# Kernel tuning notes

Hardware: AMD Instinct MI355X
Metric: run time of the kernel (lower is better)

Reference implementation:

```python
import jax, jax.numpy as jnp
import numpy as np

B, C_IN, H, W = 2, 256, 64, 64
D, NH, WS = 128, 8, 8          # embed_dim, num_heads, window_size
N_PTS = 8192
CAP = 256                      # max tokens per window (64 pixels + points, padded)
ODE_STEPS = 4                  # fixed-step RK4 approximating dopri5 on t in [0,1]


def setup_inputs() -> dict:
    key = jax.random.key(0)
    ks = jax.random.split(key, 16)
    p = lambda k, shape, fan: (jax.random.normal(k, shape, jnp.float32) / np.float32(np.sqrt(fan)))
    return {
        "in_image_feat": jax.random.normal(ks[0], (B, C_IN, H, W), jnp.float32),
        "pts_uv": jax.random.randint(ks[1], (N_PTS, 3), 0, 64),
        "pts_feat": jax.random.normal(ks[2], (N_PTS, D), jnp.float32),
        "conv_in_w": p(ks[3], (D, C_IN), C_IN),         # conv256_128 (1x1)
        "conv_in_b": jnp.zeros((D,), jnp.float32),
        "qkv_w": p(ks[4], (3 * D, D), D),               # sptr attn qkv
        "qkv_b": jnp.zeros((3 * D,), jnp.float32),
        "attnproj_w": p(ks[5], (D, D), D),              # sptr attn out proj
        "attnproj_b": jnp.zeros((D,), jnp.float32),
        "ode_w": p(ks[6], (D, D), D),                   # outimagefc128_128_ode
        "ode_b": jnp.zeros((D,), jnp.float32),
        "conv_out_w": p(ks[7], (C_IN, D), D),           # conv128_256 (1x1)
        "conv_out_b": jnp.zeros((C_IN,), jnp.float32),
    }


def _windowed_attention(feat, wid, NW, qkv_w, qkv_b, proj_w, proj_b):
    """Var-length windowed MHSA (sptr.VarLengthMultiheadSA) via pad-to-CAP."""
    T, d = feat.shape
    hd = d // NH
    order = jnp.argsort(wid)                      # stable sort by window id
    wid_s, feat_s = wid[order], feat[order]
    counts = jax.ops.segment_sum(jnp.ones_like(wid), wid, num_segments=NW)
    starts = jnp.cumsum(counts) - counts
    rank = jnp.arange(T) - starts[wid_s]          # within-window position
    valid = rank < CAP
    wid_w = jnp.where(valid, wid_s, NW)           # overflow -> dummy window
    rank_w = jnp.where(valid, rank, 0)
    buf = jnp.zeros((NW + 1, CAP, d), feat.dtype).at[wid_w, rank_w].set(feat_s)
    msk = jnp.zeros((NW + 1, CAP), bool).at[wid_w, rank_w].set(valid)
    qkv = buf @ qkv_w.T + qkv_b                   # [NW+1, CAP, 3d]
    q, k, v = (t.reshape(NW + 1, CAP, NH, hd) for t in jnp.split(qkv, 3, axis=-1))
    scores = jnp.einsum('wqhd,wkhd->whqk', q, k) / np.float32(np.sqrt(hd))
    scores = jnp.where(msk[:, None, None, :], scores, jnp.float32(-1e9))
    attn = jax.nn.softmax(scores, axis=-1)
    o = jnp.einsum('whqk,wkhd->wqhd', attn, v).reshape(NW + 1, CAP, d)
    o = o @ proj_w.T + proj_b
    out_s = jnp.where(valid[:, None], o[wid_w, rank_w], feat_s)
    return jnp.zeros_like(out_s).at[order].set(out_s)  # unsort


def reference(in_image_feat, pts_uv, pts_feat, conv_in_w, conv_in_b,
              qkv_w, qkv_b, attnproj_w, attnproj_b,
              ode_w, ode_b, conv_out_w, conv_out_b):
    b, c, h, w = in_image_feat.shape
    d = conv_in_w.shape[0]
    # 1x1 conv 256->128
    x = jnp.einsum('bchw,ec->bhwe', in_image_feat, conv_in_w) + conv_in_b
    pix_feat = x.reshape(b * h * w, d)
    # pixel uv grid (convert_image_to_uv): flatten order (b, h, w); u=w idx, v=h idx
    vv, uu = jnp.meshgrid(jnp.arange(h), jnp.arange(w), indexing='ij')
    pix_b = jnp.repeat(jnp.arange(b), h * w)
    pix_u = jnp.tile(uu.reshape(-1), b)
    pix_v = jnp.tile(vv.reshape(-1), b)
    # projected point uv (convert_pts_to_uv result, made in-range)
    pts_b = pts_uv[:, 0] % b
    pts_u = pts_uv[:, 1] % w
    pts_v = pts_uv[:, 2] % h
    tok_b = jnp.concatenate([pix_b, pts_b])
    tok_u = jnp.concatenate([pix_u, pts_u])
    tok_v = jnp.concatenate([pix_v, pts_v])
    feat = jnp.concatenate([pix_feat, pts_feat], axis=0)
    nwx, nwy = w // WS, h // WS
    wid = (tok_b * nwy + tok_v // WS) * nwx + tok_u // WS
    NW = b * nwx * nwy
    out = _windowed_attention(feat, wid, NW, qkv_w, qkv_b, attnproj_w, attnproj_b)
    img = out[: b * h * w]
    # fcode branch: odeint(ODEFunc(Linear), t=[0,1]) ~ fixed-step RK4, + residual
    f = lambda y: jax.nn.relu(y @ ode_w.T + ode_b)
    dt = jnp.float32(1.0 / ODE_STEPS)
    y = img
    for _ in range(ODE_STEPS):
        k1 = f(y); k2 = f(y + 0.5 * dt * k1); k3 = f(y + 0.5 * dt * k2); k4 = f(y + dt * k3)
        y = y + (dt / 6.0) * (k1 + 2.0 * k2 + 2.0 * k3 + k4)
    img = y + img
    # 1x1 conv 128->256 back to image layout
    img = img.reshape(b, h, w, d)
    return jnp.einsum('bhwd,cd->bchw', img, conv_out_w) + conv_out_b[None, :, None, None]
```

## Files before the change

kernel.cpp:

```cpp
#include <hip/hip_runtime.h>

typedef short bf16x8 __attribute__((ext_vector_type(8)));
typedef float f32x4 __attribute__((ext_vector_type(4)));

__device__ __forceinline__ float b2f(unsigned short s) {
    union { float f; unsigned u; } x; x.u = ((unsigned)s) << 16; return x.f;
}
__device__ __forceinline__ unsigned short f2b(float f) {
    unsigned u = __float_as_uint(f);
    unsigned r = (u + 0x7fffu + ((u >> 16) & 1u)) >> 16;
    return (unsigned short)r;
}

__global__ __launch_bounds__(256) void cast_k(const float* __restrict__ ciw,
                                              const float* __restrict__ qw,
                                              const float* __restrict__ pw,
                                              const float* __restrict__ ow,
                                              const float* __restrict__ cw,
                                              const float* __restrict__ ptsf,
                                              unsigned short* __restrict__ dst,
                                              int* __restrict__ cnt) {
    if (blockIdx.x == 0 && threadIdx.x < 128) cnt[threadIdx.x] = 0;
    int i = blockIdx.x * 256 + threadIdx.x;
    float v;
    if (i < 32768)        v = ciw[i];
    else if (i < 81920)   v = qw[i - 32768];
    else if (i < 98304)   v = pw[i - 81920];
    else if (i < 114688)  v = ow[i - 98304];
    else if (i < 147456)  v = cw[i - 114688];
    else                  v = ptsf[i - 147456];
    dst[i] = f2b(v);
}

__global__ __launch_bounds__(256) void transpose_k(const float* __restrict__ in,
                                                   unsigned short* __restrict__ out) {
    __shared__ unsigned short t[64][65];
    int p0 = blockIdx.x * 64, c0 = blockIdx.y * 64, b = blockIdx.z;
    int lane = threadIdx.x & 63, quad = threadIdx.x >> 6;
#pragma unroll
    for (int i = 0; i < 16; ++i) {
        int c = quad + i * 4;
        t[c][lane] = f2b(in[((size_t)(b * 256 + c0 + c)) * 4096 + p0 + lane]);
    }
    __syncthreads();
#pragma unroll
    for (int i = 0; i < 16; ++i) {
        int p = quad + i * 4;
        out[((size_t)(b * 4096 + p0 + p)) * 256 + c0 + lane] = t[lane][p];
    }
}

__global__ __launch_bounds__(256) void assign_k(const int* __restrict__ uv,
                                                int* __restrict__ cnt,
                                                int* __restrict__ wpts) {
    int i = blockIdx.x * 256 + threadIdx.x;
    if (i >= 8192) return;
    int b = uv[3 * i] & 1;
    int u = uv[3 * i + 1] & 63;
    int v = uv[3 * i + 2] & 63;
    int w = b * 64 + ((v >> 3) << 3) + (u >> 3);
    int slot = atomicAdd(cnt + w, 1);
    if (slot < 192) wpts[w * 192 + slot] = i;
}

template<int K, int MODE>
__global__ __launch_bounds__(256) void gemm_k(const unsigned short* __restrict__ A0,
                                              const unsigned short* __restrict__ A1,
                                              const unsigned short* __restrict__ Wm,
                                              const float* __restrict__ bias,
                                              void* __restrict__ Cv, int ldc) {
    int lane = threadIdx.x & 63;
    int wv = threadIdx.x >> 6;
    int m0 = (blockIdx.x * 4 + wv) * 16;
    int q = lane & 15, g = lane >> 4;
    const unsigned short* Arow;
    {
        int row = m0 + q;
        Arow = (A1 != nullptr && row >= 8192) ? (A1 + (size_t)(row - 8192) * K)
                                              : (A0 + (size_t)row * K);
    }
    int nb = blockIdx.y * 64;
    int koff = g * 8;
    f32x4 acc[4];
#pragma unroll
    for (int t = 0; t < 4; ++t) acc[t] = (f32x4){0.f, 0.f, 0.f, 0.f};
#pragma unroll
    for (int k0 = 0; k0 < K; k0 += 32) {
        bf16x8 a = *(const bf16x8*)(Arow + k0 + koff);
#pragma unroll
        for (int t = 0; t < 4; ++t) {
            const unsigned short* wr = Wm + (size_t)(nb + t * 16 + q) * K + k0 + koff;
            bf16x8 bfr = *(const bf16x8*)wr;
            acc[t] = __builtin_amdgcn_mfma_f32_16x16x32_bf16(a, bfr, acc[t], 0, 0, 0);
        }
    }
#pragma unroll
    for (int t = 0; t < 4; ++t) {
        int n = nb + t * 16 + q;
        float bs = bias[n];
        if constexpr (MODE == 2) {
            int p = m0 + g * 4;
            float4 pk;
            pk.x = acc[t][0] + bs;
            pk.y = acc[t][1] + bs;
            pk.z = acc[t][2] + bs;
            pk.w = acc[t][3] + bs;
            size_t ad = ((size_t)((p >> 12) * 256 + n)) * 4096 + (size_t)(p & 4095);
            *(float4*)((float*)Cv + ad) = pk;
        } else {
#pragma unroll
            for (int rr = 0; rr < 4; ++rr) {
                float v = acc[t][rr] + bs;
                int row = m0 + g * 4 + rr;
                if constexpr (MODE == 0)
                    ((unsigned short*)Cv)[(size_t)row * ldc + n] = f2b(v);
                else
                    ((float*)Cv)[(size_t)row * ldc + n] = v;
            }
        }
    }
}

__global__ __launch_bounds__(256) void attn_k(const unsigned short* __restrict__ qkv,
                                              const int* __restrict__ cnt,
                                              const int* __restrict__ wpts,
                                              unsigned short* __restrict__ aout) {
    __shared__ unsigned short Kl[256][24];
    __shared__ unsigned short Vt[16][264];
    int blk = blockIdx.x;
    int w = blk >> 3, h = blk & 7;
    int b = w >> 6, wy = (w >> 3) & 7, wx = w & 7;
    int tid = threadIdx.x, wave = tid >> 6, lane = tid & 63;
    int q = lane & 15, g = lane >> 4;
    int c = cnt[w]; if (c > 192) c = 192;
    int T = 64 + c;

    {
        int t = tid;
        if (t < T) {
            int tok;
            if (t < 64) tok = b * 4096 + (wy * 8 + (t >> 3)) * 64 + wx * 8 + (t & 7);
            else        tok = 8192 + wpts[w * 192 + t - 64];
            const unsigned short* base = qkv + (size_t)tok * 384 + h * 16;
            bf16x8 k0 = *(const bf16x8*)(base + 128);
            bf16x8 v0 = *(const bf16x8*)(base + 256);
            *(bf16x8*)&Kl[t][0] = k0;
#pragma unroll
            for (int d = 0; d < 8; ++d) Vt[d][t] = (unsigned short)v0[d];
            bf16x8 k1 = *(const bf16x8*)(base + 136);
            bf16x8 v1 = *(const bf16x8*)(base + 264);
            *(bf16x8*)&Kl[t][8] = k1;
#pragma unroll
            for (int d = 0; d < 8; ++d) Vt[8 + d][t] = (unsigned short)v1[d];
        } else {
            bf16x8 z;
#pragma unroll
            for (int d = 0; d < 8; ++d) z[d] = 0;
            *(bf16x8*)&Kl[t][0] = z;
            *(bf16x8*)&Kl[t][8] = z;
#pragma unroll
            for (int d = 0; d < 16; ++d) Vt[d][t] = 0;
        }
    }

    int qq = wave * 16 + q;
    int qrow = b * 4096 + (wy * 8 + (qq >> 3)) * 64 + wx * 8 + (qq & 7);
    bf16x8 qfrag;
#pragma unroll
    for (int j = 0; j < 8; ++j) qfrag[j] = 0;
    if (g < 2) qfrag = *(const bf16x8*)(qkv + (size_t)qrow * 384 + h * 16 + g * 8);

    __syncthreads();

    float p[16][4];
    int MT = (T + 15) >> 4;
#pragma unroll
    for (int mt = 0; mt < 16; ++mt) {
        if (mt < MT) {
            bf16x8 af = *(const bf16x8*)&Kl[mt * 16 + q][(g & 1) * 8];
            f32x4 cc = (f32x4){0.f, 0.f, 0.f, 0.f};
            cc = __builtin_amdgcn_mfma_f32_16x16x32_bf16(af, qfrag, cc, 0, 0, 0);
#pragma unroll
            for (int r = 0; r < 4; ++r) {
                int tok = mt * 16 + g * 4 + r;
                p[mt][r] = (tok < T) ? cc[r] * 0.25f : -1e30f;
            }
        } else {
#pragma unroll
            for (int r = 0; r < 4; ++r) p[mt][r] = -1e30f;
        }
    }

    float mv = -3.0e38f;
#pragma unroll
    for (int mt = 0; mt < 16; ++mt)
#pragma unroll
        for (int r = 0; r < 4; ++r) mv = fmaxf(mv, p[mt][r]);
    mv = fmaxf(mv, __shfl_xor(mv, 16));
    mv = fmaxf(mv, __shfl_xor(mv, 32));
    float ls = 0.f;
#pragma unroll
    for (int mt = 0; mt < 16; ++mt)
#pragma unroll
        for (int r = 0; r < 4; ++r) {
            float e = __expf(p[mt][r] - mv);
            p[mt][r] = e;
            ls += e;
        }
    ls += __shfl_xor(ls, 16);
    ls += __shfl_xor(ls, 32);

    f32x4 oacc = (f32x4){0.f, 0.f, 0.f, 0.f};
    int KS = (T + 31) >> 5;
    int srcA = q + (((2 * g) & 3) << 4);
    int srcB = q + (((2 * g + 1) & 3) << 4);
#pragma unroll
    for (int ks = 0; ks < 8; ++ks) {
        if (ks < KS) {
            int n0lo, n0hi, n1lo, n1hi;
            asm("v_cvt_pk_bf16_f32 %0, %1, %2" : "=v"(n0lo) : "v"(p[2 * ks][0]), "v"(p[2 * ks][1]));
            asm("v_cvt_pk_bf16_f32 %0, %1, %2" : "=v"(n0hi) : "v"(p[2 * ks][2]), "v"(p[2 * ks][3]));
            asm("v_cvt_pk_bf16_f32 %0, %1, %2" : "=v"(n1lo) : "v"(p[2 * ks + 1][0]), "v"(p[2 * ks + 1][1]));
            asm("v_cvt_pk_bf16_f32 %0, %1, %2" : "=v"(n1hi) : "v"(p[2 * ks + 1][2]), "v"(p[2 * ks + 1][3]));
            int a0 = __shfl(n0lo, srcA), b0 = __shfl(n1lo, srcA);
            int a1 = __shfl(n0hi, srcA), b1 = __shfl(n1hi, srcA);
            int a2 = __shfl(n0lo, srcB), b2 = __shfl(n1lo, srcB);
            int a3 = __shfl(n0hi, srcB), b3 = __shfl(n1hi, srcB);
            union { int d[4]; bf16x8 v; } pb;
            bool lo2 = (g < 2);
            pb.d[0] = lo2 ? a0 : b0;
            pb.d[1] = lo2 ? a1 : b1;
            pb.d[2] = lo2 ? a2 : b2;
            pb.d[3] = lo2 ? a3 : b3;
            bf16x8 vf = *(const bf16x8*)&Vt[q][ks * 32 + g * 8];
            oacc = __builtin_amdgcn_mfma_f32_16x16x32_bf16(vf, pb.v, oacc, 0, 0, 0);
        }
    }

    float inv = 1.0f / ls;
    ushort4 st;
    st.x = f2b(oacc[0] * inv);
    st.y = f2b(oacc[1] * inv);
    st.z = f2b(oacc[2] * inv);
    st.w = f2b(oacc[3] * inv);
    *(ushort4*)(aout + (size_t)qrow * 128 + h * 16 + g * 4) = st;
}

__global__ __launch_bounds__(128) void ode_k(const float* __restrict__ img,
                                             const unsigned short* __restrict__ Wg,
                                             const float* __restrict__ bg,
                                             unsigned short* __restrict__ outimg) {
    __shared__ unsigned short Wl[128][136];
    __shared__ unsigned short tc[2][16][136];
    int tid = threadIdx.x, wave = tid >> 6, lane = tid & 63;
    int g = lane >> 4, q = lane & 15;
    {
        int part = tid & 15;
#pragma unroll
        for (int it = 0; it < 16; ++it) {
            int rr = (tid >> 4) + it * 8;
            *(bf16x8*)&Wl[rr][part * 8] = *(const bf16x8*)(Wg + rr * 128 + part * 8);
        }
    }
    int R0 = blockIdx.x * 32 + wave * 16;
    float bs[8];
#pragma unroll
    for (int tn = 0; tn < 8; ++tn) bs[tn] = bg[tn * 16 + q];
    float y[32], acc[32], ko[32];
#pragma unroll
    for (int tn = 0; tn < 8; ++tn)
#pragma unroll
        for (int rr = 0; rr < 4; ++rr)
            y[tn * 4 + rr] = img[(size_t)(R0 + g * 4 + rr) * 128 + tn * 16 + q];

#define WRITE_TC(EXPR)                                            \
    {                                                             \
        _Pragma("unroll")                                         \
        for (int tn = 0; tn < 8; ++tn) {                          \
            _Pragma("unroll")                                     \
            for (int rr = 0; rr < 4; ++rr) {                      \
                int i_ = tn * 4 + rr;                             \
                tc[wave][g * 4 + rr][tn * 16 + q] = f2b(EXPR);    \
            }                                                     \
        }                                                         \
        __syncthreads();                                          \
    }

#define EVAL()                                                                         \
    {                                                                                  \
        bf16x8 af[4];                                                                  \
        _Pragma("unroll")                                                              \
        for (int tk = 0; tk < 4; ++tk)                                                 \
            af[tk] = *(const bf16x8*)&tc[wave][q][tk * 32 + g * 8];                    \
        _Pragma("unroll")                                                              \
        for (int tn = 0; tn < 8; ++tn) {                                               \
            f32x4 cc = (f32x4){0.f, 0.f, 0.f, 0.f};                                    \
            _Pragma("unroll")                                                          \
            for (int tk = 0; tk < 4; ++tk) {                                           \
                bf16x8 bfr = *(const bf16x8*)&Wl[tn * 16 + q][tk * 32 + g * 8];        \
                cc = __builtin_amdgcn_mfma_f32_16x16x32_bf16(af[tk], bfr, cc, 0, 0, 0);\
            }                                                                          \
            _Pragma("unroll")                                                          \
            for (int rr = 0; rr < 4; ++rr)                                             \
                ko[tn * 4 + rr] = fmaxf(cc[rr] + bs[tn], 0.f);                         \
        }                                                                              \
    }

    WRITE_TC(y[i_])
    const float dt = 0.25f;
    for (int st = 0; st < 4; ++st) {
        EVAL();
#pragma unroll
        for (int i = 0; i < 32; ++i) acc[i] = y[i] + (dt / 6.f) * ko[i];
        WRITE_TC(y[i_] + (0.5f * dt) * ko[i_])
        EVAL();
#pragma unroll
        for (int i = 0; i < 32; ++i) acc[i] += (dt / 3.f) * ko[i];
        WRITE_TC(y[i_] + (0.5f * dt) * ko[i_])
        EVAL();
#pragma unroll
        for (int i = 0; i < 32; ++i) acc[i] += (dt / 3.f) * ko[i];
        WRITE_TC(y[i_] + dt * ko[i_])
        EVAL();
#pragma unroll
        for (int i = 0; i < 32; ++i) y[i] = acc[i] + (dt / 6.f) * ko[i];
        WRITE_TC(y[i_])
    }
#pragma unroll
    for (int tn = 0; tn < 8; ++tn)
#pragma unroll
        for (int rr = 0; rr < 4; ++rr) {
            size_t idx = (size_t)(R0 + g * 4 + rr) * 128 + tn * 16 + q;
            outimg[idx] = f2b(y[tn * 4 + rr] + img[idx]);
        }
#undef WRITE_TC
#undef EVAL
}

extern "C" void kernel_launch(void* const* d_in, const int* in_sizes, int n_in,
                              void* d_out, int out_size, void* d_ws, size_t ws_size,
                              hipStream_t stream) {
    (void)in_sizes; (void)n_in; (void)out_size; (void)ws_size;
    const float* img_in = (const float*)d_in[0];
    const int*   pts_uv = (const int*)d_in[1];
    const float* ptsf   = (const float*)d_in[2];
    const float* ciw    = (const float*)d_in[3];
    const float* cib    = (const float*)d_in[4];
    const float* qw     = (const float*)d_in[5];
    const float* qb     = (const float*)d_in[6];
    const float* pw     = (const float*)d_in[7];
    const float* pb     = (const float*)d_in[8];
    const float* ow     = (const float*)d_in[9];
    const float* ob     = (const float*)d_in[10];
    const float* cw     = (const float*)d_in[11];
    const float* cb     = (const float*)d_in[12];

    char* ws = (char*)d_ws;
    unsigned short* Arm  = (unsigned short*)(ws);
    unsigned short* feat = (unsigned short*)(ws + 4194304);
    unsigned short* qkv  = (unsigned short*)(ws + 6291456);
    unsigned short* aout = (unsigned short*)(ws + 18874368);
    float*          img0 = (float*)(ws + 20971520);
    unsigned short* imgf = (unsigned short*)(ws + 25165824);
    int*            cnt  = (int*)(ws + 27262976);
    int*            wpts = (int*)(ws + 27263488);
    unsigned short* wb   = (unsigned short*)(ws + 27787264);
    unsigned short* ciw_b = wb;
    unsigned short* qw_b  = wb + 32768;
    unsigned short* pw_b  = wb + 81920;
    unsigned short* ow_b  = wb + 98304;
    unsigned short* cw_b  = wb + 114688;
    unsigned short* ptsf_b= wb + 147456;

    cast_k<<<4672, 256, 0, stream>>>(ciw, qw, pw, ow, cw, ptsf, wb, cnt);
    transpose_k<<<dim3(64, 4, 2), 256, 0, stream>>>(img_in, Arm);
    assign_k<<<32, 256, 0, stream>>>(pts_uv, cnt, wpts);
    gemm_k<256, 0><<<dim3(128, 2), 256, 0, stream>>>(Arm, nullptr, ciw_b, cib, feat, 128);
    gemm_k<128, 0><<<dim3(256, 6), 256, 0, stream>>>(feat, ptsf_b, qw_b, qb, qkv, 384);
    attn_k<<<1024, 256, 0, stream>>>(qkv, cnt, wpts, aout);
    gemm_k<128, 1><<<dim3(128, 2), 256, 0, stream>>>(aout, nullptr, pw_b, pb, img0, 128);
    ode_k<<<256, 128, 0, stream>>>(img0, ow_b, ob, imgf);
    gemm_k<128, 2><<<dim3(128, 4), 256, 0, stream>>>(imgf, nullptr, cw_b, cb, d_out, 0);
}
```

Measured before the change: 170.5 us.

## Fuse transpose into conv-in GEMM and fuse proj+ODE+conv-out into one tail kernel

Folds the NCHW-to-row transpose into the input 1x1 conv kernel through shared memory, converts point features to bf16 inside the QKV GEMM instead of in a separate cast pass, and merges the attention output projection, the RK4 ODE and the output 1x1 conv into a single per-row-block kernel. This removes several launches and the intermediate global buffers (transposed image, fp32 img0, bf16 imgf). In exchange the fused kernels run fewer blocks (128 and 256) and carry more registers, which can lower occupancy. Tail-kernel weights are read directly from global memory.

```diff
diff --git a/kernel.cpp b/kernel.cpp
--- a/kernel.cpp
+++ b/kernel.cpp
@@ -17,7 +17,6 @@
                                               const float* __restrict__ pw,
                                               const float* __restrict__ ow,
                                               const float* __restrict__ cw,
-                                              const float* __restrict__ ptsf,
                                               unsigned short* __restrict__ dst,
                                               int* __restrict__ cnt) {
     if (blockIdx.x == 0 && threadIdx.x < 128) cnt[threadIdx.x] = 0;
@@ -27,27 +26,8 @@
     else if (i < 81920)   v = qw[i - 32768];
     else if (i < 98304)   v = pw[i - 81920];
     else if (i < 114688)  v = ow[i - 98304];
-    else if (i < 147456)  v = cw[i - 114688];
-    else                  v = ptsf[i - 147456];
+    else                  v = cw[i - 114688];
     dst[i] = f2b(v);
-}
-
-__global__ __launch_bounds__(256) void transpose_k(const float* __restrict__ in,
-                                                   unsigned short* __restrict__ out) {
-    __shared__ unsigned short t[64][65];
-    int p0 = blockIdx.x * 64, c0 = blockIdx.y * 64, b = blockIdx.z;
-    int lane = threadIdx.x & 63, quad = threadIdx.x >> 6;
-#pragma unroll
-    for (int i = 0; i < 16; ++i) {
-        int c = quad + i * 4;
-        t[c][lane] = f2b(in[((size_t)(b * 256 + c0 + c)) * 4096 + p0 + lane]);
-    }
-    __syncthreads();
-#pragma unroll
-    for (int i = 0; i < 16; ++i) {
-        int p = quad + i * 4;
-        out[((size_t)(b * 4096 + p0 + p)) * 256 + c0 + lane] = t[lane][p];
-    }
 }
 
 __global__ __launch_bounds__(256) void assign_k(const int* __restrict__ uv,
@@ -63,61 +43,93 @@
     if (slot < 192) wpts[w * 192 + slot] = i;
 }
 
-template<int K, int MODE>
-__global__ __launch_bounds__(256) void gemm_k(const unsigned short* __restrict__ A0,
-                                              const unsigned short* __restrict__ A1,
-                                              const unsigned short* __restrict__ Wm,
-                                              const float* __restrict__ bias,
-                                              void* __restrict__ Cv, int ldc) {
-    int lane = threadIdx.x & 63;
-    int wv = threadIdx.x >> 6;
+__global__ __launch_bounds__(256) void cin_k(const float* __restrict__ in,
+                                             const unsigned short* __restrict__ Wm,
+                                             const float* __restrict__ bias,
+                                             unsigned short* __restrict__ feat) {
+    __shared__ unsigned short t[64][65];
+    __shared__ unsigned short At[64][264];
+    int p0 = blockIdx.x * 64, b = p0 >> 12, hw0 = p0 & 4095;
+    int lane = threadIdx.x & 63, quad = threadIdx.x >> 6;
+    for (int j = 0; j < 4; ++j) {
+        int c0 = j * 64;
+#pragma unroll
+        for (int i = 0; i < 16; ++i) {
+            int c = quad + i * 4;
+            t[c][lane] = f2b(in[((size_t)(b * 256 + c0 + c)) * 4096 + hw0 + lane]);
+        }
+        __syncthreads();
+#pragma unroll
+        for (int i = 0; i < 16; ++i) {
+            int p = quad + i * 4;
+            At[p][c0 + lane] = t[lane][p];
+        }
+        __syncthreads();
+    }
+    int q = lane & 15, g = lane >> 4;
+    int m0 = quad * 16;
+    f32x4 acc[8];
+#pragma unroll
+    for (int tn = 0; tn < 8; ++tn) acc[tn] = (f32x4){0.f, 0.f, 0.f, 0.f};
+#pragma unroll
+    for (int k0 = 0; k0 < 256; k0 += 32) {
+        bf16x8 a = *(const bf16x8*)&At[m0 + q][k0 + g * 8];
+#pragma unroll
+        for (int tn = 0; tn < 8; ++tn) {
+            bf16x8 bfr = *(const bf16x8*)(Wm + (size_t)(tn * 16 + q) * 256 + k0 + g * 8);
+            acc[tn] = __builtin_amdgcn_mfma_f32_16x16x32_bf16(a, bfr, acc[tn], 0, 0, 0);
+        }
+    }
+#pragma unroll
+    for (int tn = 0; tn < 8; ++tn) {
+        int n = tn * 16 + q;
+        float bs = bias[n];
+#pragma unroll
+        for (int rr = 0; rr < 4; ++rr)
+            feat[(size_t)(p0 + m0 + g * 4 + rr) * 128 + n] = f2b(acc[tn][rr] + bs);
+    }
+}
+
+__global__ __launch_bounds__(256) void qkv_k(const unsigned short* __restrict__ feat,
+                                             const float* __restrict__ ptsf,
+                                             const unsigned short* __restrict__ Wm,
+                                             const float* __restrict__ bias,
+                                             unsigned short* __restrict__ qkv) {
+    int lane = threadIdx.x & 63, wv = threadIdx.x >> 6;
     int m0 = (blockIdx.x * 4 + wv) * 16;
     int q = lane & 15, g = lane >> 4;
-    const unsigned short* Arow;
-    {
-        int row = m0 + q;
-        Arow = (A1 != nullptr && row >= 8192) ? (A1 + (size_t)(row - 8192) * K)
-                                              : (A0 + (size_t)row * K);
-    }
-    int nb = blockIdx.y * 64;
-    int koff = g * 8;
+    int nb = blockIdx.y * 64, koff = g * 8;
+    bool isPt = m0 >= 8192;
     f32x4 acc[4];
 #pragma unroll
-    for (int t = 0; t < 4; ++t) acc[t] = (f32x4){0.f, 0.f, 0.f, 0.f};
-#pragma unroll
-    for (int k0 = 0; k0 < K; k0 += 32) {
-        bf16x8 a = *(const bf16x8*)(Arow + k0 + koff);
-#pragma unroll
-        for (int t = 0; t < 4; ++t) {
-            const unsigned short* wr = Wm + (size_t)(nb + t * 16 + q) * K + k0 + koff;
-            bf16x8 bfr = *(const bf16x8*)wr;
-            acc[t] = __builtin_amdgcn_mfma_f32_16x16x32_bf16(a, bfr, acc[t], 0, 0, 0);
-        }
-    }
-#pragma unroll
-    for (int t = 0; t < 4; ++t) {
-        int n = nb + t * 16 + q;
+    for (int tt = 0; tt < 4; ++tt) acc[tt] = (f32x4){0.f, 0.f, 0.f, 0.f};
+#pragma unroll
+    for (int k0 = 0; k0 < 128; k0 += 32) {
+        bf16x8 a;
+        if (isPt) {
+            const float* pr = ptsf + (size_t)(m0 + q - 8192) * 128 + k0 + koff;
+            float4 f0 = *(const float4*)pr;
+            float4 f1 = *(const float4*)(pr + 4);
+            a[0] = (short)f2b(f0.x); a[1] = (short)f2b(f0.y);
+            a[2] = (short)f2b(f0.z); a[3] = (short)f2b(f0.w);
+            a[4] = (short)f2b(f1.x); a[5] = (short)f2b(f1.y);
+            a[6] = (short)f2b(f1.z); a[7] = (short)f2b(f1.w);
+        } else {
+            a = *(const bf16x8*)(feat + (size_t)(m0 + q) * 128 + k0 + koff);
+        }
+#pragma unroll
+        for (int tt = 0; tt < 4; ++tt) {
+            bf16x8 bfr = *(const bf16x8*)(Wm + (size_t)(nb + tt * 16 + q) * 128 + k0 + koff);
+            acc[tt] = __builtin_amdgcn_mfma_f32_16x16x32_bf16(a, bfr, acc[tt], 0, 0, 0);
+        }
+    }
+#pragma unroll
+    for (int tt = 0; tt < 4; ++tt) {
+        int n = nb + tt * 16 + q;
         float bs = bias[n];
-        if constexpr (MODE == 2) {
-            int p = m0 + g * 4;
-            float4 pk;
-            pk.x = acc[t][0] + bs;
-            pk.y = acc[t][1] + bs;
-            pk.z = acc[t][2] + bs;
-            pk.w = acc[t][3] + bs;
-            size_t ad = ((size_t)((p >> 12) * 256 + n)) * 4096 + (size_t)(p & 4095);
-            *(float4*)((float*)Cv + ad) = pk;
-        } else {
-#pragma unroll
-            for (int rr = 0; rr < 4; ++rr) {
-                float v = acc[t][rr] + bs;
-                int row = m0 + g * 4 + rr;
-                if constexpr (MODE == 0)
-                    ((unsigned short*)Cv)[(size_t)row * ldc + n] = f2b(v);
-                else
-                    ((float*)Cv)[(size_t)row * ldc + n] = v;
-            }
-        }
+#pragma unroll
+        for (int rr = 0; rr < 4; ++rr)
+            qkv[(size_t)(m0 + g * 4 + rr) * 384 + n] = f2b(acc[tt][rr] + bs);
     }
 }
 
@@ -134,7 +146,6 @@
     int q = lane & 15, g = lane >> 4;
     int c = cnt[w]; if (c > 192) c = 192;
     int T = 64 + c;
-
     {
         int t = tid;
         if (t < T) {
@@ -162,7 +173,6 @@
             for (int d = 0; d < 16; ++d) Vt[d][t] = 0;
         }
     }
-
     int qq = wave * 16 + q;
     int qrow = b * 4096 + (wy * 8 + (qq >> 3)) * 64 + wx * 8 + (qq & 7);
     bf16x8 qfrag;
@@ -190,7 +200,6 @@
             for (int r = 0; r < 4; ++r) p[mt][r] = -1e30f;
         }
     }
-
     float mv = -3.0e38f;
 #pragma unroll
     for (int mt = 0; mt < 16; ++mt)
@@ -236,7 +245,6 @@
             oacc = __builtin_amdgcn_mfma_f32_16x16x32_bf16(vf, pb.v, oacc, 0, 0, 0);
         }
     }
-
     float inv = 1.0f / ls;
     ushort4 st;
     st.x = f2b(oacc[0] * inv);
@@ -246,10 +254,14 @@
     *(ushort4*)(aout + (size_t)qrow * 128 + h * 16 + g * 4) = st;
 }
 
-__global__ __launch_bounds__(128) void ode_k(const float* __restrict__ img,
-                                             const unsigned short* __restrict__ Wg,
-                                             const float* __restrict__ bg,
-                                             unsigned short* __restrict__ outimg) {
+__global__ __launch_bounds__(128) void tail_k(const unsigned short* __restrict__ aout,
+                                              const unsigned short* __restrict__ pwb,
+                                              const float* __restrict__ pb,
+                                              const unsigned short* __restrict__ owb,
+                                              const float* __restrict__ ob,
+                                              const unsigned short* __restrict__ cwb,
+                                              const float* __restrict__ cb,
+                                              float* __restrict__ outp) {
     __shared__ unsigned short Wl[128][136];
     __shared__ unsigned short tc[2][16][136];
     int tid = threadIdx.x, wave = tid >> 6, lane = tid & 63;
@@ -259,19 +271,40 @@
 #pragma unroll
         for (int it = 0; it < 16; ++it) {
             int rr = (tid >> 4) + it * 8;
-            *(bf16x8*)&Wl[rr][part * 8] = *(const bf16x8*)(Wg + rr * 128 + part * 8);
+            *(bf16x8*)&Wl[rr][part * 8] = *(const bf16x8*)(owb + rr * 128 + part * 8);
         }
     }
     int R0 = blockIdx.x * 32 + wave * 16;
+
+    float y0[32];
+    {
+        const unsigned short* Arow = aout + (size_t)(R0 + q) * 128;
+        f32x4 pacc[8];
+#pragma unroll
+        for (int tn = 0; tn < 8; ++tn) pacc[tn] = (f32x4){0.f, 0.f, 0.f, 0.f};
+#pragma unroll
+        for (int k0 = 0; k0 < 128; k0 += 32) {
+            bf16x8 a = *(const bf16x8*)(Arow + k0 + g * 8);
+#pragma unroll
+            for (int tn = 0; tn < 8; ++tn) {
+                bf16x8 bfr = *(const bf16x8*)(pwb + (size_t)(tn * 16 + q) * 128 + k0 + g * 8);
+                pacc[tn] = __builtin_amdgcn_mfma_f32_16x16x32_bf16(a, bfr, pacc[tn], 0, 0, 0);
+            }
+        }
+#pragma unroll
+        for (int tn = 0; tn < 8; ++tn) {
+            float bs = pb[tn * 16 + q];
+#pragma unroll
+            for (int rr = 0; rr < 4; ++rr) y0[tn * 4 + rr] = pacc[tn][rr] + bs;
+        }
+    }
+
     float bs[8];
 #pragma unroll
-    for (int tn = 0; tn < 8; ++tn) bs[tn] = bg[tn * 16 + q];
+    for (int tn = 0; tn < 8; ++tn) bs[tn] = ob[tn * 16 + q];
     float y[32], acc[32], ko[32];
 #pragma unroll
-    for (int tn = 0; tn < 8; ++tn)
-#pragma unroll
-        for (int rr = 0; rr < 4; ++rr)
-            y[tn * 4 + rr] = img[(size_t)(R0 + g * 4 + rr) * 128 + tn * 16 + q];
+    for (int i = 0; i < 32; ++i) y[i] = y0[i];
 
 #define WRITE_TC(EXPR)                                            \
     {                                                             \
@@ -326,13 +359,30 @@
         for (int i = 0; i < 32; ++i) y[i] = acc[i] + (dt / 6.f) * ko[i];
         WRITE_TC(y[i_])
     }
-#pragma unroll
-    for (int tn = 0; tn < 8; ++tn)
-#pragma unroll
-        for (int rr = 0; rr < 4; ++rr) {
-            size_t idx = (size_t)(R0 + g * 4 + rr) * 128 + tn * 16 + q;
-            outimg[idx] = f2b(y[tn * 4 + rr] + img[idx]);
-        }
+
+    WRITE_TC(y[i_] + y0[i_])
+    {
+        int p = R0 + g * 4;
+        int bb = p >> 12, plo = p & 4095;
+#pragma unroll
+        for (int tn2 = 0; tn2 < 16; ++tn2) {
+            f32x4 cc = (f32x4){0.f, 0.f, 0.f, 0.f};
+#pragma unroll
+            for (int tk = 0; tk < 4; ++tk) {
+                bf16x8 af = *(const bf16x8*)&tc[wave][q][tk * 32 + g * 8];
+                bf16x8 bfr = *(const bf16x8*)(cwb + (size_t)(tn2 * 16 + q) * 128 + tk * 32 + g * 8);
+                cc = __builtin_amdgcn_mfma_f32_16x16x32_bf16(af, bfr, cc, 0, 0, 0);
+            }
+            int ch = tn2 * 16 + q;
+            float bsv = cb[ch];
+            float4 stv;
+            stv.x = cc[0] + bsv;
+            stv.y = cc[1] + bsv;
+            stv.z = cc[2] + bsv;
+            stv.w = cc[3] + bsv;
+            *(float4*)(outp + ((size_t)(bb * 256 + ch)) * 4096 + plo) = stv;
+        }
+    }
 #undef WRITE_TC
 #undef EVAL
 }
@@ -356,29 +406,22 @@
     const float* cb     = (const float*)d_in[12];
 
     char* ws = (char*)d_ws;
-    unsigned short* Arm  = (unsigned short*)(ws);
-    unsigned short* feat = (unsigned short*)(ws + 4194304);
-    unsigned short* qkv  = (unsigned short*)(ws + 6291456);
-    unsigned short* aout = (unsigned short*)(ws + 18874368);
-    float*          img0 = (float*)(ws + 20971520);
-    unsigned short* imgf = (unsigned short*)(ws + 25165824);
-    int*            cnt  = (int*)(ws + 27262976);
-    int*            wpts = (int*)(ws + 27263488);
-    unsigned short* wb   = (unsigned short*)(ws + 27787264);
+    unsigned short* feat = (unsigned short*)(ws);
+    unsigned short* qkv  = (unsigned short*)(ws + 2097152);
+    unsigned short* aout = (unsigned short*)(ws + 14680064);
+    int*            cnt  = (int*)(ws + 16777216);
+    int*            wpts = (int*)(ws + 16777728);
+    unsigned short* wb   = (unsigned short*)(ws + 16876544);
     unsigned short* ciw_b = wb;
     unsigned short* qw_b  = wb + 32768;
     unsigned short* pw_b  = wb + 81920;
     unsigned short* ow_b  = wb + 98304;
     unsigned short* cw_b  = wb + 114688;
-    unsigned short* ptsf_b= wb + 147456;
-
-    cast_k<<<4672, 256, 0, stream>>>(ciw, qw, pw, ow, cw, ptsf, wb, cnt);
-    transpose_k<<<dim3(64, 4, 2), 256, 0, stream>>>(img_in, Arm);
+
+    cast_k<<<576, 256, 0, stream>>>(ciw, qw, pw, ow, cw, wb, cnt);
     assign_k<<<32, 256, 0, stream>>>(pts_uv, cnt, wpts);
-    gemm_k<256, 0><<<dim3(128, 2), 256, 0, stream>>>(Arm, nullptr, ciw_b, cib, feat, 128);
-    gemm_k<128, 0><<<dim3(256, 6), 256, 0, stream>>>(feat, ptsf_b, qw_b, qb, qkv, 384);
+    cin_k<<<128, 256, 0, stream>>>(img_in, ciw_b, cib, feat);
+    qkv_k<<<dim3(256, 6), 256, 0, stream>>>(feat, ptsf, qw_b, qb, qkv);
     attn_k<<<1024, 256, 0, stream>>>(qkv, cnt, wpts, aout);
-    gemm_k<128, 1><<<dim3(128, 2), 256, 0, stream>>>(aout, nullptr, pw_b, pb, img0, 128);
-    ode_k<<<256, 128, 0, stream>>>(img0, ow_b, ob, imgf);
-    gemm_k<128, 2><<<dim3(128, 4), 256, 0, stream>>>(imgf, nullptr, cw_b, cb, d_out, 0);
-}
+    tail_k<<<256, 128, 0, stream>>>(aout, pw_b, pb, ow_b, ob, cw_b, cb, (float*)d_out);
+}
```

After: 170.8 us. No clear change (+0.2%).
